# Performance work log

Hardware: AMD Instinct MI355X
Metric: run time of the kernel (lower is better)

## Reference

```python
import jax, jax.numpy as jnp
import numpy as np

NEG_SLOPE = 0.2  # PyG GATConv default negative_slope
EPS = 1e-16


def gat_conv(x, src, dst, num_nodes, W, a_src, a_dst, bias, heads, out_c, concat):
    """PyG-style GATConv (eval mode, self-loops already appended).
    x: [N, F_in]; src/dst: [E] (edge j->i with src=j, dst=i).
    W: [F_in, heads*out_c]; a_src/a_dst: [heads, out_c]; bias: [heads*out_c] or [out_c].
    """
    xw = (x @ W).reshape(num_nodes, heads, out_c)          # [N, H, C]
    alpha_src = jnp.sum(xw * a_src, axis=-1)               # [N, H]
    alpha_dst = jnp.sum(xw * a_dst, axis=-1)               # [N, H]
    e = jax.nn.leaky_relu(alpha_src[src] + alpha_dst[dst], NEG_SLOPE)  # [E, H]
    # numerically stable segment softmax over edges grouped by destination node
    m = jax.ops.segment_max(e, dst, num_segments=num_nodes)            # [N, H]
    e = jnp.exp(e - m[dst])
    denom = jax.ops.segment_sum(e, dst, num_segments=num_nodes)        # [N, H]
    alpha = e / (denom[dst] + EPS)                                     # [E, H]
    # weighted scatter-sum aggregation of source messages
    out = jax.ops.segment_sum(xw[src] * alpha[:, :, None], dst, num_segments=num_nodes)  # [N, H, C]
    if concat:
        out = out.reshape(num_nodes, heads * out_c)
    else:
        out = out.mean(axis=1)
    return out + bias


def setup_inputs() -> dict:
    key = jax.random.key(0)
    ks = jax.random.split(key, 12)
    N, E = 50000, 800000
    F_in, Hid, H1, Out = 512, 32, 8, 64

    def xavier(k, shape, gain=1.414):
        fan_in, fan_out = shape[0], shape[-1] if len(shape) == 2 else int(np.prod(shape[1:]))
        a = gain * np.sqrt(6.0 / (fan_in + fan_out))
        return jax.random.uniform(k, shape, jnp.float32, -a, a)

    x = jax.random.normal(ks[0], (N, F_in), jnp.float32)
    edge_index = jax.random.randint(ks[1], (2, E), 0, N, jnp.int64)

    W1 = xavier(ks[2], (F_in, H1 * Hid))
    a_src1 = xavier(ks[3], (H1, Hid))
    a_dst1 = xavier(ks[4], (H1, Hid))
    b1 = jnp.zeros((H1 * Hid,), jnp.float32)

    W2 = xavier(ks[5], (H1 * Hid, Out))
    a_src2 = xavier(ks[6], (1, Out))
    a_dst2 = xavier(ks[7], (1, Out))
    b2 = jnp.zeros((Out,), jnp.float32)

    return {"x": x, "edge_index": edge_index,
            "W1": W1, "a_src1": a_src1, "a_dst1": a_dst1, "b1": b1,
            "W2": W2, "a_src2": a_src2, "a_dst2": a_dst2, "b2": b2}


def reference(x, edge_index, W1, a_src1, a_dst1, b1, W2, a_src2, a_dst2, b2):
    N = x.shape[0]
    # add self-loops (PyG GATConv default add_self_loops=True)
    loop = jnp.arange(N, dtype=edge_index.dtype)
    src = jnp.concatenate([edge_index[0], loop])
    dst = jnp.concatenate([edge_index[1], loop])

    # eval mode: all dropouts are identity
    h = gat_conv(x, src, dst, N, W1, a_src1, a_dst1, b1, heads=8, out_c=32, concat=True)
    h = jax.nn.elu(h)
    h = gat_conv(h, src, dst, N, W2, a_src2, a_dst2, b2, heads=1, out_c=64, concat=False)
    return jax.nn.log_softmax(h, axis=1)
```

## Files before the change

kernel.cpp:

```cpp
#include <hip/hip_runtime.h>
#include <hip/hip_bf16.h>


typedef __attribute__((ext_vector_type(8)))  __bf16          bf16x8;
typedef __attribute__((ext_vector_type(8)))  unsigned short  ushort8;
typedef __attribute__((ext_vector_type(16))) float           f32x16;
typedef __attribute__((ext_vector_type(2)))  float           f32x2;

#define NEG_SLOPE 0.2f
#define EPS_GAT 1e-16f

static __device__ __forceinline__ float lrelu(float x) {
    return x > 0.0f ? x : NEG_SLOPE * x;
}
static __device__ __forceinline__ unsigned short f2bf(float f) {
    unsigned u = __float_as_uint(f);
    return (unsigned short)((u + 0x7fffu + ((u >> 16) & 1u)) >> 16);
}
static __device__ __forceinline__ float bf2f(unsigned short v) {
    return __uint_as_float(((unsigned)v) << 16);
}
static __device__ __forceinline__ unsigned encf(float x) {
    unsigned u = __float_as_uint(x);
    return (u >> 31) ? ~u : (u | 0x80000000u);
}
static __device__ __forceinline__ float decf(unsigned e) {
    unsigned u = (e >> 31) ? (e & 0x7fffffffu) : ~e;
    return __uint_as_float(u);
}

__global__ void k_hist_w(const void* __restrict__ eix, int* __restrict__ counts,
                         int E, int EB,
                         const float* __restrict__ W1, const float* __restrict__ W2,
                         unsigned short* __restrict__ w1t, unsigned short* __restrict__ w2t) {
    int b = blockIdx.x;
    if (b < EB) {
        int i = b * 256 + threadIdx.x;
        unsigned w = ((const unsigned*)eix)[2 * min(i, E - 1) + 1];
        bool is64 = (__syncthreads_or((int)(w != 0u)) == 0);
        if (i < E) {
            int d = is64 ? (int)((const long long*)eix)[E + i]
                         : ((const int*)eix)[E + i];
            atomicAdd(&counts[d], 1);
        }
    } else {
        int t = (b - EB) * 256 + threadIdx.x;
        if (t < 512 * 256) {
            int k = t >> 8, m = t & 255;
            w1t[m * 512 + k] = f2bf(W1[t]);
        } else {
            int u = t - 512 * 256;
            if (u < 256 * 64) {
                int k = u >> 6, m = u & 63;
                w2t[m * 256 + k] = f2bf(W2[u]);
            }
        }
    }
}

__global__ void k_scan1(const int* __restrict__ counts, int* __restrict__ rowp,
                        int* __restrict__ bsum, int N) {
    __shared__ int s[256];
    int t = threadIdx.x, i = blockIdx.x * 256 + t;
    int v = (i < N) ? counts[i] : 0;
    s[t] = v;
    __syncthreads();
    for (int off = 1; off < 256; off <<= 1) {
        int u = (t >= off) ? s[t - off] : 0;
        __syncthreads();
        s[t] += u;
        __syncthreads();
    }
    if (i < N) rowp[i] = s[t] - v;
    if (t == 255) bsum[blockIdx.x] = s[255];
}

__global__ void k_scan2(const int* __restrict__ bsum, int* __restrict__ boff,
                        int* __restrict__ rowp_last, int NB) {
    __shared__ int s[256];
    int t = threadIdx.x;
    int v = (t < NB) ? bsum[t] : 0;
    s[t] = v;
    __syncthreads();
    for (int off = 1; off < 256; off <<= 1) {
        int u = (t >= off) ? s[t - off] : 0;
        __syncthreads();
        s[t] += u;
        __syncthreads();
    }
    if (t < NB) boff[t] = s[t] - v;
    if (t == 255) *rowp_last = s[255];
}

__global__ void k_scan3(int* __restrict__ rowp, int* __restrict__ cursor,
                        const int* __restrict__ boff, int N) {
    int i = blockIdx.x * 256 + threadIdx.x;
    if (i < N) {
        int r = rowp[i] + boff[blockIdx.x];
        rowp[i] = r;
        cursor[i] = r;
    }
}

__global__ void k_fill(const void* __restrict__ eix, int* __restrict__ cursor,
                       int* __restrict__ ssrc, int E) {
    int i = blockIdx.x * 256 + threadIdx.x;
    unsigned w = ((const unsigned*)eix)[2 * min(i, E - 1) + 1];
    bool is64 = (__syncthreads_or((int)(w != 0u)) == 0);
    if (i >= E) return;
    int s, d;
    if (is64) {
        s = (int)((const long long*)eix)[i];
        d = (int)((const long long*)eix)[E + i];
    } else {
        s = ((const int*)eix)[i];
        d = ((const int*)eix)[E + i];
    }
    int pos = atomicAdd(&cursor[d], 1);
    ssrc[pos] = s;
}

template <int BM, int BN, int NT, bool AF32, bool OUTBF>
__global__ __launch_bounds__(NT) void k_gemm(const void* __restrict__ Ain,
                                             const unsigned short* __restrict__ Bt,
                                             void* __restrict__ Cout, int Nrows, int K) {
    constexpr int LD = 40;
    constexpr int AIT = BM * 4 / NT;
    constexpr int BIT = BN * 4 / NT;
    __shared__ __align__(16) unsigned short As[BM * LD];
    __shared__ __align__(16) unsigned short Bs[BN * LD];
    const int tid = threadIdx.x;
    const int blockRow = blockIdx.x * BM;
    const int wave = tid >> 6, lane = tid & 63;
    constexpr int WR = BM / 64;
    const int wr = wave % WR, wc = wave / WR;
    const int m = lane & 31;
    const int ksel = (lane >> 5) * 8;

    f32x16 acc00{}, acc01{}, acc10{}, acc11{};

    float4  af0[AIT], af1[AIT];
    ushort8 ab[AIT];
    ushort8 bb[BIT];

    auto loadA = [&](int kt) {
        #pragma unroll
        for (int i = 0; i < AIT; ++i) {
            int idx = tid + i * NT;
            int r = idx >> 2, kc = (idx & 3) * 8;
            int grow = blockRow + r;
            if constexpr (AF32) {
                const float* A = (const float*)Ain;
                if (grow < Nrows) {
                    const float* ap = A + (size_t)grow * K + kt + kc;
                    af0[i] = *(const float4*)ap;
                    af1[i] = *(const float4*)(ap + 4);
                } else {
                    af0[i] = make_float4(0.f, 0.f, 0.f, 0.f);
                    af1[i] = make_float4(0.f, 0.f, 0.f, 0.f);
                }
            } else {
                const unsigned short* A = (const unsigned short*)Ain;
                ushort8 o{};
                if (grow < Nrows) o = *(const ushort8*)(A + (size_t)grow * K + kt + kc);
                ab[i] = o;
            }
        }
    };
    auto loadB = [&](int kt) {
        #pragma unroll
        for (int i = 0; i < BIT; ++i) {
            int idx = tid + i * NT;
            int r = idx >> 2, kc = (idx & 3) * 8;
            bb[i] = *(const ushort8*)(Bt + (size_t)r * K + kt + kc);
        }
    };
    auto writeAB = [&]() {
        #pragma unroll
        for (int i = 0; i < AIT; ++i) {
            int idx = tid + i * NT;
            int r = idx >> 2, kc = (idx & 3) * 8;
            if constexpr (AF32) {
                union { ushort8 u; __hip_bfloat162 h[4]; } cv;
                cv.h[0] = __float22bfloat162_rn(make_float2(af0[i].x, af0[i].y));
                cv.h[1] = __float22bfloat162_rn(make_float2(af0[i].z, af0[i].w));
                cv.h[2] = __float22bfloat162_rn(make_float2(af1[i].x, af1[i].y));
                cv.h[3] = __float22bfloat162_rn(make_float2(af1[i].z, af1[i].w));
                *(ushort8*)&As[r * LD + kc] = cv.u;
            } else {
                *(ushort8*)&As[r * LD + kc] = ab[i];
            }
        }
        #pragma unroll
        for (int i = 0; i < BIT; ++i) {
            int idx = tid + i * NT;
            int r = idx >> 2, kc = (idx & 3) * 8;
            *(ushort8*)&Bs[r * LD + kc] = bb[i];
        }
    };

    loadA(0);
    loadB(0);
    for (int kt = 0; kt < K; kt += 32) {
        writeAB();
        __syncthreads();
        if (kt + 32 < K) {
            loadA(kt + 32);
            loadB(kt + 32);
        }
        #pragma unroll
        for (int kk = 0; kk < 32; kk += 16) {
            bf16x8 a0 = *(const bf16x8*)&As[(wr * 64 +      m) * LD + kk + ksel];
            bf16x8 a1 = *(const bf16x8*)&As[(wr * 64 + 32 + m) * LD + kk + ksel];
            bf16x8 b0 = *(const bf16x8*)&Bs[(wc * 64 +      m) * LD + kk + ksel];
            bf16x8 b1 = *(const bf16x8*)&Bs[(wc * 64 + 32 + m) * LD + kk + ksel];
            acc00 = __builtin_amdgcn_mfma_f32_32x32x16_bf16(a0, b0, acc00, 0, 0, 0);
            acc01 = __builtin_amdgcn_mfma_f32_32x32x16_bf16(a0, b1, acc01, 0, 0, 0);
            acc10 = __builtin_amdgcn_mfma_f32_32x32x16_bf16(a1, b0, acc10, 0, 0, 0);
            acc11 = __builtin_amdgcn_mfma_f32_32x32x16_bf16(a1, b1, acc11, 0, 0, 0);
        }
        __syncthreads();
    }

    const int dcol = wc * 64 + (lane & 31);
    const int dquad = 4 * (lane >> 5);
    auto store_tile = [&](const f32x16& a, int rt, int ct) {
        #pragma unroll
        for (int r = 0; r < 16; ++r) {
            int row = blockRow + wr * 64 + rt * 32 + (r & 3) + 8 * (r >> 2) + dquad;
            if (row < Nrows) {
                size_t off = (size_t)row * BN + dcol + ct * 32;
                if constexpr (OUTBF) ((unsigned short*)Cout)[off] = f2bf(a[r]);
                else                 ((float*)Cout)[off] = a[r];
            }
        }
    };
    store_tile(acc00, 0, 0); store_tile(acc01, 0, 1);
    store_tile(acc10, 1, 0); store_tile(acc11, 1, 1);
}

__global__ void k_alpha(const unsigned short* __restrict__ xw, const float* __restrict__ a_s,
                        const float* __restrict__ a_d, float* __restrict__ os,
                        float* __restrict__ od, unsigned* __restrict__ Menc,
                        int NH, int H, int C) {
    __shared__ float red[256];
    int t = blockIdx.x * 256 + threadIdx.x;
    float s = -1e30f, d = 0.f;
    if (t < NH) {
        int n = t / H, h = t - n * H;
        const unsigned short* row = xw + (size_t)n * H * C + h * C;
        s = 0.f;
        for (int c = 0; c < C; c += 8) {
            ushort8 v = *(const ushort8*)(row + c);
            #pragma unroll
            for (int q = 0; q < 8; ++q) {
                float f = bf2f(v[q]);
                s += f * a_s[h * C + c + q];
                d += f * a_d[h * C + c + q];
            }
        }
        os[t] = s; od[t] = d;
    }
    red[threadIdx.x] = s;
    __syncthreads();
    for (int off = 128; off >= H; off >>= 1) {
        if (threadIdx.x < off) red[threadIdx.x] = fmaxf(red[threadIdx.x], red[threadIdx.x + off]);
        __syncthreads();
    }
    if ((int)threadIdx.x < H) atomicMax(&Menc[threadIdx.x], encf(red[threadIdx.x]));
}

__global__ __launch_bounds__(256, 6) void k_agg_l1(
        const unsigned short* __restrict__ xw1, const float* __restrict__ asrc,
        const float* __restrict__ adst, const unsigned* __restrict__ Menc,
        const float* __restrict__ b1, const int* __restrict__ rp,
        const int* __restrict__ ssrc, unsigned short* __restrict__ hbf, int N) {
    int wid = (blockIdx.x * 256 + threadIdx.x) >> 6;
    if (wid >= N) return;
    const int lane = threadIdx.x & 63;
    const int g  = lane >> 4;
    const int q  = lane & 15;
    const int f0 = q * 16;
    const int h  = q >> 1;
    const int ih = wid * 8 + h;
    const float ad = adst[ih];
    const float m  = lrelu(decf(Menc[h]) + ad);
    f32x2 acc[8];
    float s;
    {
        float w = (g == 0) ? __expf(lrelu(asrc[ih] + ad) - m) : 0.0f;
        const unsigned short* pr = xw1 + (size_t)wid * 256 + f0;
        ushort8 lo = *(const ushort8*)pr;
        ushort8 hi = *(const ushort8*)(pr + 8);
        s = w;
        const unsigned* dl = (const unsigned*)&lo;
        const unsigned* dh = (const unsigned*)&hi;
        #pragma unroll
        for (int p = 0; p < 4; ++p) {
            acc[p].x     = w * __uint_as_float(dl[p] << 16);
            acc[p].y     = w * __uint_as_float(dl[p] & 0xffff0000u);
            acc[4 + p].x = w * __uint_as_float(dh[p] << 16);
            acc[4 + p].y = w * __uint_as_float(dh[p] & 0xffff0000u);
        }
    }
    const int e0 = rp[wid], e1 = rp[wid + 1];
    if (e0 < e1) {
        const int NQ = (e1 - e0 + 3) >> 2;

        auto LDJ = [&](int base, int& j, bool& v) {
            v = base + g < e1;
            j = ssrc[min(base + g, e1 - 1)];
        };
        auto LDD = [&](int j, float& as, ushort8& lo, ushort8& hi) {
            as = asrc[j * 8 + h];
            const unsigned short* p = xw1 + ((size_t)j << 8) + f0;
            lo = *(const ushort8*)p;
            hi = *(const ushort8*)(p + 8);
        };
        auto CONS = [&](bool v, float as, const ushort8& lo, const ushort8& hi) {
            float w = v ? __expf(lrelu(as + ad) - m) : 0.0f;
            s += w;
            f32x2 wp; wp.x = w; wp.y = w;
            const unsigned* dl = (const unsigned*)&lo;
            const unsigned* dh = (const unsigned*)&hi;
            #pragma unroll
            for (int p = 0; p < 4; ++p) {
                f32x2 x;
                x.x = __uint_as_float(dl[p] << 16);
                x.y = __uint_as_float(dl[p] & 0xffff0000u);
                asm("v_pk_fma_f32 %0, %1, %2, %3"
                    : "=v"(acc[p]) : "v"(x), "v"(wp), "v"(acc[p]));
            }
            #pragma unroll
            for (int p = 0; p < 4; ++p) {
                f32x2 x;
                x.x = __uint_as_float(dh[p] << 16);
                x.y = __uint_as_float(dh[p] & 0xffff0000u);
                asm("v_pk_fma_f32 %0, %1, %2, %3"
                    : "=v"(acc[4 + p]) : "v"(x), "v"(wp), "v"(acc[4 + p]));
            }
        };

        int j0, j1, j2, j3, j4; bool v0, v1, v2, v3, v4;
        float as0, as1, as2;
        ushort8 lo0, hi0, lo1, hi1, lo2, hi2;
        LDJ(e0,      j0, v0);
        LDJ(e0 + 4,  j1, v1);
        LDJ(e0 + 8,  j2, v2);
        LDD(j0, as0, lo0, hi0);
        LDJ(e0 + 12, j3, v3);
        LDD(j1, as1, lo1, hi1);
        LDJ(e0 + 16, j4, v4);
        LDD(j2, as2, lo2, hi2);

        #pragma unroll 2
        for (int k = 0; k < NQ - 3; ++k) {
            int jN; bool vN;
            LDJ(e0 + 4 * k + 20, jN, vN);
            float as3; ushort8 lo3, hi3;
            LDD(j3, as3, lo3, hi3);
            CONS(v0, as0, lo0, hi0);
            v0 = v1; as0 = as1; lo0 = lo1; hi0 = hi1;
            v1 = v2; as1 = as2; lo1 = lo2; hi1 = hi2;
            v2 = v3; as2 = as3; lo2 = lo3; hi2 = hi3;
            v3 = v4; j3 = j4;
            v4 = vN; j4 = jN;
        }
        CONS(v0, as0, lo0, hi0);
        CONS(v1, as1, lo1, hi1);
        CONS(v2, as2, lo2, hi2);
    }
    s += __shfl_xor(s, 16, 64);
    s += __shfl_xor(s, 32, 64);
    #pragma unroll
    for (int p = 0; p < 8; ++p) {
        acc[p].x += __shfl_xor(acc[p].x, 16, 64);
        acc[p].x += __shfl_xor(acc[p].x, 32, 64);
        acc[p].y += __shfl_xor(acc[p].y, 16, 64);
        acc[p].y += __shfl_xor(acc[p].y, 32, 64);
    }
    float inv = 1.0f / (s + EPS_GAT);
    f32x2 p0 = (g & 2) ? ((g & 1) ? acc[6] : acc[4]) : ((g & 1) ? acc[2] : acc[0]);
    f32x2 p1 = (g & 2) ? ((g & 1) ? acc[7] : acc[5]) : ((g & 1) ? acc[3] : acc[1]);
    int fw = f0 + g * 4;
    float vv[4] = { p0.x, p0.y, p1.x, p1.y };
    ushort4 o;
    #pragma unroll
    for (int i = 0; i < 4; ++i) {
        float v = vv[i] * inv + b1[fw + i];
        v = v > 0.f ? v : expm1f(v);
        ((unsigned short*)&o)[i] = f2bf(v);
    }
    *(ushort4*)(hbf + (size_t)wid * 256 + fw) = o;
}

__global__ __launch_bounds__(256, 6) void k_agg_l2(
        const unsigned short* __restrict__ xw2, const float* __restrict__ asrc,
        const float* __restrict__ adst, const unsigned* __restrict__ Menc,
        const float* __restrict__ b2, const int* __restrict__ rp,
        const int* __restrict__ ssrc, float* __restrict__ out, int N) {
    int wid = (blockIdx.x * 256 + threadIdx.x) >> 6;
    if (wid >= N) return;
    const int lane = threadIdx.x & 63;
    const int g  = lane >> 3;
    const int q  = lane & 7;
    const int f0 = q * 8;
    const float ad = adst[wid];
    const float m = lrelu(decf(Menc[0]) + ad);
    f32x2 acc[4];
    float s;
    {
        float w = (g == 0) ? __expf(lrelu(asrc[wid] + ad) - m) : 0.0f;
        ushort8 xv = *(const ushort8*)(xw2 + (size_t)wid * 64 + f0);
        s = w;
        const unsigned* dx = (const unsigned*)&xv;
        #pragma unroll
        for (int p = 0; p < 4; ++p) {
            acc[p].x = w * __uint_as_float(dx[p] << 16);
            acc[p].y = w * __uint_as_float(dx[p] & 0xffff0000u);
        }
    }
    const int e0 = rp[wid], e1 = rp[wid + 1];
    if (e0 < e1) {
        const int NQ = (e1 - e0 + 7) >> 3;

        auto LDJ = [&](int base, int& j, bool& v) {
            v = base + g < e1;
            j = ssrc[min(base + g, e1 - 1)];
        };
        auto LDD = [&](int j, float& as, ushort8& xv) {
            as = asrc[j];
            xv = *(const ushort8*)(xw2 + ((size_t)j << 6) + f0);
        };
        auto CONS = [&](bool v, float as, const ushort8& xv) {
            float w = v ? __expf(lrelu(as + ad) - m) : 0.0f;
            s += w;
            f32x2 wp; wp.x = w; wp.y = w;
            const unsigned* dx = (const unsigned*)&xv;
            #pragma unroll
            for (int p = 0; p < 4; ++p) {
                f32x2 x;
                x.x = __uint_as_float(dx[p] << 16);
                x.y = __uint_as_float(dx[p] & 0xffff0000u);
                asm("v_pk_fma_f32 %0, %1, %2, %3"
                    : "=v"(acc[p]) : "v"(x), "v"(wp), "v"(acc[p]));
            }
        };

        int j0, j1, j2, j3; bool v0, v1, v2, v3;
        float as0, as1; ushort8 xv0, xv1;
        LDJ(e0,      j0, v0);
        LDJ(e0 + 8,  j1, v1);
        LDD(j0, as0, xv0);
        LDJ(e0 + 16, j2, v2);
        LDD(j1, as1, xv1);
        LDJ(e0 + 24, j3, v3);

        #pragma unroll 2
        for (int k = 0; k < NQ - 2; ++k) {
            int jN; bool vN;
            LDJ(e0 + 8 * k + 32, jN, vN);
            float as2; ushort8 xv2;
            LDD(j2, as2, xv2);
            CONS(v0, as0, xv0);
            v0 = v1; as0 = as1; xv0 = xv1;
            v1 = v2; as1 = as2; xv1 = xv2;
            v2 = v3; j2 = j3;
            v3 = vN; j3 = jN;
        }
        CONS(v0, as0, xv0);
        if (NQ >= 2) CONS(v1, as1, xv1);
    }
    s += __shfl_xor(s, 8, 64);
    s += __shfl_xor(s, 16, 64);
    s += __shfl_xor(s, 32, 64);
    #pragma unroll
    for (int p = 0; p < 4; ++p) {
        acc[p].x += __shfl_xor(acc[p].x, 8, 64);
        acc[p].x += __shfl_xor(acc[p].x, 16, 64);
        acc[p].x += __shfl_xor(acc[p].x, 32, 64);
        acc[p].y += __shfl_xor(acc[p].y, 8, 64);
        acc[p].y += __shfl_xor(acc[p].y, 16, 64);
        acc[p].y += __shfl_xor(acc[p].y, 32, 64);
    }
    float inv = 1.0f / (s + EPS_GAT);
    float val[8];
    float mx = -1e30f;
    #pragma unroll
    for (int i = 0; i < 8; ++i) {
        float a = (i & 1) ? acc[i >> 1].y : acc[i >> 1].x;
        val[i] = a * inv + b2[f0 + i];
        mx = fmaxf(mx, val[i]);
    }
    #pragma unroll
    for (int off = 4; off > 0; off >>= 1) mx = fmaxf(mx, __shfl_xor(mx, off, 64));
    float sm = 0.f;
    #pragma unroll
    for (int i = 0; i < 8; ++i) sm += __expf(val[i] - mx);
    #pragma unroll
    for (int off = 4; off > 0; off >>= 1) sm += __shfl_xor(sm, off, 64);
    float lse = mx + logf(sm);
    if (g == 0) {
        float4 o0 = make_float4(val[0] - lse, val[1] - lse, val[2] - lse, val[3] - lse);
        float4 o1 = make_float4(val[4] - lse, val[5] - lse, val[6] - lse, val[7] - lse);
        *(float4*)(out + (size_t)wid * 64 + f0)     = o0;
        *(float4*)(out + (size_t)wid * 64 + f0 + 4) = o1;
    }
}

static inline int cdiv(int a, int b) { return (a + b - 1) / b; }

extern "C" void kernel_launch(void* const* d_in, const int* in_sizes, int n_in,
                              void* d_out, int out_size, void* d_ws, size_t ws_size,
                              hipStream_t stream) {
    const float* x   = (const float*)d_in[0];
    const void*  eix = d_in[1];
    const float* W1  = (const float*)d_in[2];
    const float* as1 = (const float*)d_in[3];
    const float* ad1 = (const float*)d_in[4];
    const float* b1  = (const float*)d_in[5];
    const float* W2  = (const float*)d_in[6];
    const float* as2 = (const float*)d_in[7];
    const float* ad2 = (const float*)d_in[8];
    const float* b2  = (const float*)d_in[9];
    float* out = (float*)d_out;

    const int N = in_sizes[0] / 512;
    const int E = in_sizes[1] / 2;
    const int EB = cdiv(E, 256);
    const int WB = cdiv(512 * 256 + 256 * 64, 256);
    const int NB = cdiv(N, 256);
    const int NB1 = cdiv(N * 8, 256);
    const int NB2 = cdiv(N, 256);
    (void)n_in; (void)out_size; (void)ws_size;

    char* base = (char*)d_ws;
    size_t o = 0;
    auto alloc = [&](size_t bytes) -> char* {
        o = (o + 255) & ~(size_t)255;
        char* p = base + o;
        o += bytes;
        return p;
    };
    unsigned short* xw1b  = (unsigned short*)alloc((size_t)N * 256 * 2);
    unsigned short* hbf   = (unsigned short*)alloc((size_t)N * 256 * 2);
    unsigned short* xw2b  = (unsigned short*)alloc((size_t)N * 64 * 2);
    float*          asrc1 = (float*)alloc((size_t)N * 8 * 4);
    float*          adst1 = (float*)alloc((size_t)N * 8 * 4);
    float*          asrc2 = (float*)alloc((size_t)N * 4);
    float*          adst2 = (float*)alloc((size_t)N * 4);
    size_t zero_begin = (o + 255) & ~(size_t)255;
    unsigned*       Menc  = (unsigned*)alloc(16 * 4);
    int*            counts= (int*)alloc((size_t)N * 4);
    size_t zero_end = o;
    int*            cursor= (int*)alloc((size_t)N * 4);
    int*            rowp  = (int*)alloc((size_t)(N + 1) * 4);
    int*            bsum  = (int*)alloc(256 * 4);
    int*            boff  = (int*)alloc(256 * 4);
    unsigned short* w1t   = (unsigned short*)alloc(512 * 256 * 2);
    unsigned short* w2t   = (unsigned short*)alloc(256 * 64 * 2);
    int*            ssrc  = (int*)alloc((size_t)E * 4);

    hipMemsetAsync(base + zero_begin, 0, zero_end - zero_begin, stream);

    k_hist_w<<<EB + WB, 256, 0, stream>>>(eix, counts, E, EB, W1, W2, w1t, w2t);
    k_scan1<<<NB, 256, 0, stream>>>(counts, rowp, bsum, N);
    k_scan2<<<1, 256, 0, stream>>>(bsum, boff, rowp + N, NB);
    k_scan3<<<NB, 256, 0, stream>>>(rowp, cursor, boff, N);
    k_fill<<<EB, 256, 0, stream>>>(eix, cursor, ssrc, E);

    k_gemm<128, 256, 512, true, true><<<cdiv(N, 128), 512, 0, stream>>>(x, w1t, xw1b, N, 512);
    k_alpha<<<NB1, 256, 0, stream>>>(xw1b, as1, ad1, asrc1, adst1, Menc, N * 8, 8, 32);
    k_agg_l1<<<cdiv(N * 64, 256), 256, 0, stream>>>(xw1b, asrc1, adst1, Menc, b1,
                                                    rowp, ssrc, hbf, N);
    k_gemm<256, 64, 256, false, true><<<cdiv(N, 256), 256, 0, stream>>>(hbf, w2t, xw2b, N, 256);
    k_alpha<<<NB2, 256, 0, stream>>>(xw2b, as2, ad2, asrc2, adst2, Menc + 8, N, 1, 64);
    k_agg_l2<<<cdiv(N * 64, 256), 256, 0, stream>>>(xw2b, asrc2, adst2, Menc + 8, b2,
                                                    rowp, ssrc, out, N);
}
```

Before: 417.0 us.

## Split layer-1 aggregation into two feature-half launches

The layer-1 aggregation kernel now handles only 128 of the 256 features per launch, selected by a new half argument, and is launched twice. Each lane loads one 16-byte vector per neighbour instead of two, which halves the accumulator registers and the gathered working set per pass. The aim is to raise occupancy and make the gathered xw1 half fit better in cache. The cost is that edge indices and alpha values are read twice, an extra launch is added, and only a quarter of the lanes do the final write.

New measurement: 431.9 us. 1.04x slower.

```diff
diff --git a/kernel.cpp b/kernel.cpp
--- a/kernel.cpp
+++ b/kernel.cpp
@@ -274,33 +274,29 @@
         const unsigned short* __restrict__ xw1, const float* __restrict__ asrc,
         const float* __restrict__ adst, const unsigned* __restrict__ Menc,
         const float* __restrict__ b1, const int* __restrict__ rp,
-        const int* __restrict__ ssrc, unsigned short* __restrict__ hbf, int N) {
+        const int* __restrict__ ssrc, unsigned short* __restrict__ hbf,
+        int N, int half) {
     int wid = (blockIdx.x * 256 + threadIdx.x) >> 6;
     if (wid >= N) return;
     const int lane = threadIdx.x & 63;
     const int g  = lane >> 4;
     const int q  = lane & 15;
-    const int f0 = q * 16;
-    const int h  = q >> 1;
+    const int fb = half * 128 + q * 8;
+    const int h  = fb >> 5;
     const int ih = wid * 8 + h;
     const float ad = adst[ih];
     const float m  = lrelu(decf(Menc[h]) + ad);
-    f32x2 acc[8];
+    f32x2 acc[4];
     float s;
     {
         float w = (g == 0) ? __expf(lrelu(asrc[ih] + ad) - m) : 0.0f;
-        const unsigned short* pr = xw1 + (size_t)wid * 256 + f0;
-        ushort8 lo = *(const ushort8*)pr;
-        ushort8 hi = *(const ushort8*)(pr + 8);
+        ushort8 xv = *(const ushort8*)(xw1 + (size_t)wid * 256 + fb);
         s = w;
-        const unsigned* dl = (const unsigned*)&lo;
-        const unsigned* dh = (const unsigned*)&hi;
+        const unsigned* dx = (const unsigned*)&xv;
         #pragma unroll
         for (int p = 0; p < 4; ++p) {
-            acc[p].x     = w * __uint_as_float(dl[p] << 16);
-            acc[p].y     = w * __uint_as_float(dl[p] & 0xffff0000u);
-            acc[4 + p].x = w * __uint_as_float(dh[p] << 16);
-            acc[4 + p].y = w * __uint_as_float(dh[p] & 0xffff0000u);
+            acc[p].x = w * __uint_as_float(dx[p] << 16);
+            acc[p].y = w * __uint_as_float(dx[p] & 0xffff0000u);
         }
     }
     const int e0 = rp[wid], e1 = rp[wid + 1];
@@ -311,87 +307,77 @@
             v = base + g < e1;
             j = ssrc[min(base + g, e1 - 1)];
         };
-        auto LDD = [&](int j, float& as, ushort8& lo, ushort8& hi) {
+        auto LDD = [&](int j, float& as, ushort8& xv) {
             as = asrc[j * 8 + h];
-            const unsigned short* p = xw1 + ((size_t)j << 8) + f0;
-            lo = *(const ushort8*)p;
-            hi = *(const ushort8*)(p + 8);
+            xv = *(const ushort8*)(xw1 + ((size_t)j << 8) + fb);
         };
-        auto CONS = [&](bool v, float as, const ushort8& lo, const ushort8& hi) {
+        auto CONS = [&](bool v, float as, const ushort8& xv) {
             float w = v ? __expf(lrelu(as + ad) - m) : 0.0f;
             s += w;
             f32x2 wp; wp.x = w; wp.y = w;
-            const unsigned* dl = (const unsigned*)&lo;
-            const unsigned* dh = (const unsigned*)&hi;
+            const unsigned* dx = (const unsigned*)&xv;
             #pragma unroll
             for (int p = 0; p < 4; ++p) {
                 f32x2 x;
-                x.x = __uint_as_float(dl[p] << 16);
-                x.y = __uint_as_float(dl[p] & 0xffff0000u);
+                x.x = __uint_as_float(dx[p] << 16);
+                x.y = __uint_as_float(dx[p] & 0xffff0000u);
                 asm("v_pk_fma_f32 %0, %1, %2, %3"
                     : "=v"(acc[p]) : "v"(x), "v"(wp), "v"(acc[p]));
             }
-            #pragma unroll
-            for (int p = 0; p < 4; ++p) {
-                f32x2 x;
-                x.x = __uint_as_float(dh[p] << 16);
-                x.y = __uint_as_float(dh[p] & 0xffff0000u);
-                asm("v_pk_fma_f32 %0, %1, %2, %3"
-                    : "=v"(acc[4 + p]) : "v"(x), "v"(wp), "v"(acc[4 + p]));
-            }
         };
 
         int j0, j1, j2, j3, j4; bool v0, v1, v2, v3, v4;
         float as0, as1, as2;
-        ushort8 lo0, hi0, lo1, hi1, lo2, hi2;
+        ushort8 d0, d1, d2;
         LDJ(e0,      j0, v0);
         LDJ(e0 + 4,  j1, v1);
         LDJ(e0 + 8,  j2, v2);
-        LDD(j0, as0, lo0, hi0);
+        LDD(j0, as0, d0);
         LDJ(e0 + 12, j3, v3);
-        LDD(j1, as1, lo1, hi1);
+        LDD(j1, as1, d1);
         LDJ(e0 + 16, j4, v4);
-        LDD(j2, as2, lo2, hi2);
+        LDD(j2, as2, d2);
 
         #pragma unroll 2
         for (int k = 0; k < NQ - 3; ++k) {
             int jN; bool vN;
             LDJ(e0 + 4 * k + 20, jN, vN);
-            float as3; ushort8 lo3, hi3;
-            LDD(j3, as3, lo3, hi3);
-            CONS(v0, as0, lo0, hi0);
-            v0 = v1; as0 = as1; lo0 = lo1; hi0 = hi1;
-            v1 = v2; as1 = as2; lo1 = lo2; hi1 = hi2;
-            v2 = v3; as2 = as3; lo2 = lo3; hi2 = hi3;
+            float as3; ushort8 d3;
+            LDD(j3, as3, d3);
+            CONS(v0, as0, d0);
+            v0 = v1; as0 = as1; d0 = d1;
+            v1 = v2; as1 = as2; d1 = d2;
+            v2 = v3; as2 = as3; d2 = d3;
             v3 = v4; j3 = j4;
             v4 = vN; j4 = jN;
         }
-        CONS(v0, as0, lo0, hi0);
-        CONS(v1, as1, lo1, hi1);
-        CONS(v2, as2, lo2, hi2);
+        CONS(v0, as0, d0);
+        CONS(v1, as1, d1);
+        CONS(v2, as2, d2);
     }
     s += __shfl_xor(s, 16, 64);
     s += __shfl_xor(s, 32, 64);
     #pragma unroll
-    for (int p = 0; p < 8; ++p) {
+    for (int p = 0; p < 4; ++p) {
         acc[p].x += __shfl_xor(acc[p].x, 16, 64);
         acc[p].x += __shfl_xor(acc[p].x, 32, 64);
         acc[p].y += __shfl_xor(acc[p].y, 16, 64);
         acc[p].y += __shfl_xor(acc[p].y, 32, 64);
     }
-    float inv = 1.0f / (s + EPS_GAT);
-    f32x2 p0 = (g & 2) ? ((g & 1) ? acc[6] : acc[4]) : ((g & 1) ? acc[2] : acc[0]);
-    f32x2 p1 = (g & 2) ? ((g & 1) ? acc[7] : acc[5]) : ((g & 1) ? acc[3] : acc[1]);
-    int fw = f0 + g * 4;
-    float vv[4] = { p0.x, p0.y, p1.x, p1.y };
-    ushort4 o;
-    #pragma unroll
-    for (int i = 0; i < 4; ++i) {
-        float v = vv[i] * inv + b1[fw + i];
-        v = v > 0.f ? v : expm1f(v);
-        ((unsigned short*)&o)[i] = f2bf(v);
-    }
-    *(ushort4*)(hbf + (size_t)wid * 256 + fw) = o;
+    if (g == 0) {
+        float inv = 1.0f / (s + EPS_GAT);
+        ushort8 o;
+        #pragma unroll
+        for (int p = 0; p < 4; ++p) {
+            float v0 = acc[p].x * inv + b1[fb + 2 * p];
+            float v1 = acc[p].y * inv + b1[fb + 2 * p + 1];
+            v0 = v0 > 0.f ? v0 : expm1f(v0);
+            v1 = v1 > 0.f ? v1 : expm1f(v1);
+            o[2 * p]     = f2bf(v0);
+            o[2 * p + 1] = f2bf(v1);
+        }
+        *(ushort8*)(hbf + (size_t)wid * 256 + fb) = o;
+    }
 }
 
 __global__ __launch_bounds__(256, 6) void k_agg_l2(
@@ -572,7 +558,9 @@
     k_gemm<128, 256, 512, true, true><<<cdiv(N, 128), 512, 0, stream>>>(x, w1t, xw1b, N, 512);
     k_alpha<<<NB1, 256, 0, stream>>>(xw1b, as1, ad1, asrc1, adst1, Menc, N * 8, 8, 32);
     k_agg_l1<<<cdiv(N * 64, 256), 256, 0, stream>>>(xw1b, asrc1, adst1, Menc, b1,
-                                                    rowp, ssrc, hbf, N);
+                                                    rowp, ssrc, hbf, N, 0);
+    k_agg_l1<<<cdiv(N * 64, 256), 256, 0, stream>>>(xw1b, asrc1, adst1, Menc, b1,
+                                                    rowp, ssrc, hbf, N, 1);
     k_gemm<256, 64, 256, false, true><<<cdiv(N, 256), 256, 0, stream>>>(hbf, w2t, xw2b, N, 256);
     k_alpha<<<NB2, 256, 0, stream>>>(xw2b, as2, ad2, asrc2, adst2, Menc + 8, N, 1, 64);
     k_agg_l2<<<cdiv(N * 64, 256), 256, 0, stream>>>(xw2b, asrc2, adst2, Menc + 8, b2,
```
